# Performance work log

Hardware: AMD Instinct MI355X
Metric: run time of the kernel (lower is better)

## Reference

```python
import jax, jax.numpy as jnp
import numpy as np

OUTPUT_LEN = 8  # init: output_len
# init: pred_conversion=False, conf_thres=None, vote_conf_by_count=True, select_by_conf=True


def setup_inputs() -> dict:
    key = jax.random.key(0)
    x = jax.random.normal(key, (128, 8192, 64), dtype=jnp.float32)
    return {"x": x}


def _per_sample(conf, pred):
    # conf, pred: [T]
    T = conf.shape[0]
    # run-length encoding (unique_consecutive): mark the start of each run
    is_start = jnp.concatenate([jnp.ones((1,), bool), pred[1:] != pred[:-1]])
    run_id = jnp.cumsum(is_start.astype(jnp.int32)) - 1  # [T], run index per position
    # count of each run (padded to T segments; unused segments are 0)
    counts = jax.ops.segment_sum(jnp.ones((T,), conf.dtype), run_id, num_segments=T)
    # voted confidence at run starts: conf_at_start * run_count (vote_conf_by_count=True)
    voted = jnp.where(is_start, conf * counts[run_id], -jnp.inf)
    # select_by_conf=True: take top output_len runs by voted confidence
    vals, idx = jax.lax.top_k(voted, OUTPUT_LEN)
    sel = pred[idx]
    # fewer runs than output_len -> pad with 0 (torch pads with new_zeros)
    sel = jnp.where(jnp.isfinite(vals), sel, 0)
    return sel


def reference(x):
    p = jax.nn.softmax(x, axis=-1)          # [B, T, C]
    conf = jnp.max(p, axis=-1)              # [B, T]
    pred = jnp.argmax(p, axis=-1)           # [B, T] int
    out = jax.vmap(_per_sample)(conf, pred)  # [B, OUTPUT_LEN] int
    return out.astype(x.dtype)               # x.new_tensor(results) -> float
```

## Files before the change

### kernel.cpp

```cpp
#include <hip/hip_runtime.h>
#include <stdint.h>

#define T_LEN 8192
#define C_LEN 64
#define OUT_LEN 8

__global__ __launch_bounds__(256) void softmax_stats_kernel(
    const float* __restrict__ x, float* __restrict__ conf,
    int* __restrict__ pred, int nrows)
{
    const int tid  = threadIdx.x;
    const int wave = tid >> 6;
    const int lane = tid & 63;
    const int rw   = lane >> 4;
    const int sub  = lane & 15;
    const long long row = (long long)blockIdx.x * 16 + wave * 4 + rw;
    if (row >= nrows) return;

    const float4 v = ((const float4*)(x + row * C_LEN))[sub];

    float m = v.x; int mi = sub * 4;
    if (v.y > m) { m = v.y; mi = sub * 4 + 1; }
    if (v.z > m) { m = v.z; mi = sub * 4 + 2; }
    if (v.w > m) { m = v.w; mi = sub * 4 + 3; }

    const unsigned int s0 = __float_as_uint(m);
    const unsigned int u0 = (s0 & 0x80000000u) ? ~s0 : (s0 | 0x80000000u);
    unsigned long long key =
        ((unsigned long long)u0 << 32) | (unsigned int)~mi;

    #pragma unroll
    for (int off = 8; off >= 1; off >>= 1) {
        const unsigned long long o = __shfl_xor(key, off);
        if (o > key) key = o;
    }

    const unsigned int uu = (unsigned int)(key >> 32);
    const float M = __uint_as_float(
        (uu & 0x80000000u) ? (uu ^ 0x80000000u) : ~uu);

    float s = __expf(v.x - M) + __expf(v.y - M)
            + __expf(v.z - M) + __expf(v.w - M);
    #pragma unroll
    for (int off = 8; off >= 1; off >>= 1) s += __shfl_xor(s, off);

    if (sub == 0) {
        conf[row] = 1.0f / s;
        pred[row] = (int)~(unsigned int)(key & 0xffffffffu);
    }
}

__global__ __launch_bounds__(256) void topk_kernel(
    const float* __restrict__ conf, const int* __restrict__ pred,
    float* __restrict__ out)
{
    __shared__ short pred_s[T_LEN];
    __shared__ float voted_s[T_LEN];
    __shared__ unsigned long long wkey[4];
    __shared__ int   dirty;
    __shared__ float outbuf[OUT_LEN];

    const int b    = blockIdx.x;
    const int tid  = threadIdx.x;
    const int lane = tid & 63, wave = tid >> 6;
    const int* __restrict__   pb = pred + (long long)b * T_LEN;
    const float* __restrict__ cb = conf + (long long)b * T_LEN;

    for (int i = tid; i < T_LEN / 4; i += 256) {
        const int4 p4 = ((const int4*)pb)[i];
        short4 q; q.x = (short)p4.x; q.y = (short)p4.y;
        q.z = (short)p4.z; q.w = (short)p4.w;
        *(short4*)&pred_s[4 * i] = q;
    }
    if (tid == 0) dirty = -1;
    __syncthreads();

    for (int t = tid; t < T_LEN; t += 256) {
        const short p = pred_s[t];
        const bool start = (t == 0) || (pred_s[t - 1] != p);
        float v = 0.0f;
        if (start) {
            int len = 1;
            while (t + len < T_LEN && pred_s[t + len] == p) ++len;
            v = cb[t] * (float)len;
        }
        voted_s[t] = v;
    }
    __syncthreads();

    for (int r = 0; r < OUT_LEN; ++r) {
        if (dirty == -1 || dirty == wave) {
            unsigned long long best = 0ull;
            const int base = wave * (T_LEN / 4);
            #pragma unroll 4
            for (int k = 0; k < T_LEN / 4 / 64; ++k) {
                const int t = base + k * 64 + lane;
                const unsigned long long key =
                    ((unsigned long long)__float_as_uint(voted_s[t]) << 32)
                    | (unsigned int)(~t);
                if (key > best) best = key;
            }
            #pragma unroll
            for (int off = 32; off >= 1; off >>= 1) {
                const unsigned long long o = __shfl_xor(best, off);
                if (o > best) best = o;
            }
            if (lane == 0) wkey[wave] = best;
        }
        __syncthreads();
        if (tid == 0) {
            unsigned long long bb = wkey[0];
            #pragma unroll
            for (int w = 1; w < 4; ++w) if (wkey[w] > bb) bb = wkey[w];
            const unsigned int widx = ~(unsigned int)(bb & 0xffffffffu);
            const float v = __uint_as_float((unsigned int)(bb >> 32));
            float ov = 0.0f;
            if (v > 0.0f) {
                ov = (float)pred_s[widx];
                voted_s[widx] = 0.0f;
                dirty = (int)(widx / (T_LEN / 4));
            } else {
                dirty = 4;
            }
            outbuf[r] = ov;
        }
        __syncthreads();
    }
    if (tid < OUT_LEN) out[b * OUT_LEN + tid] = outbuf[tid];
}

extern "C" void kernel_launch(void* const* d_in, const int* in_sizes, int n_in,
                              void* d_out, int out_size, void* d_ws, size_t ws_size,
                              hipStream_t stream) {
    const float* x = (const float*)d_in[0];
    const int total = in_sizes[0];
    const int nrows = total / C_LEN;
    const int B     = nrows / T_LEN;

    float* conf = (float*)d_ws;
    int*   pred = (int*)((char*)d_ws + (size_t)nrows * sizeof(float));
    float* out  = (float*)d_out;

    const int gridA = (nrows + 15) / 16;
    softmax_stats_kernel<<<gridA, 256, 0, stream>>>(x, conf, pred, nrows);
    softmax_stats_kernel<<<gridA, 256, 0, stream>>>(x, conf, pred, nrows);
    topk_kernel<<<B, 256, 0, stream>>>(conf, pred, out);
}
```

Before: 418.0 us.

## Split per-sample top-k into segmented blocks with merge, drop duplicate softmax launch

The softmax stats kernel, which was launched twice, now runs once and writes conf and pred packed into one int2 array. The per-sample top-k is split into four segment blocks per sample. Each block computes run-length votes with a halo plus global fallback, then emits its top-8 candidate keys. A small merge kernel picks the final top-8 per sample. This raises the top-k stage from 128 to 512 blocks and removes a redundant pass over the 256 MB input, at the cost of an extra launch and candidate buffer traffic.

```diff
diff --git a/kernel.cpp b/kernel.cpp
--- a/kernel.cpp
+++ b/kernel.cpp
@@ -4,10 +4,11 @@
 #define T_LEN 8192
 #define C_LEN 64
 #define OUT_LEN 8
+#define SEG 2048
+#define HALO 512
 
 __global__ __launch_bounds__(256) void softmax_stats_kernel(
-    const float* __restrict__ x, float* __restrict__ conf,
-    int* __restrict__ pred, int nrows)
+    const float* __restrict__ x, int2* __restrict__ packed, int nrows)
 {
     const int tid  = threadIdx.x;
     const int wave = tid >> 6;
@@ -45,59 +46,68 @@
     for (int off = 8; off >= 1; off >>= 1) s += __shfl_xor(s, off);
 
     if (sub == 0) {
-        conf[row] = 1.0f / s;
-        pred[row] = (int)~(unsigned int)(key & 0xffffffffu);
+        int2 o;
+        o.x = __float_as_int(1.0f / s);
+        o.y = (int)~(unsigned int)(key & 0xffffffffu);
+        packed[row] = o;
     }
 }
 
-__global__ __launch_bounds__(256) void topk_kernel(
-    const float* __restrict__ conf, const int* __restrict__ pred,
-    float* __restrict__ out)
+__global__ __launch_bounds__(256) void topk_seg_kernel(
+    const int2* __restrict__ packed, unsigned long long* __restrict__ cand)
 {
-    __shared__ short pred_s[T_LEN];
-    __shared__ float voted_s[T_LEN];
+    __shared__ short pred_s[SEG + HALO + 1];
+    __shared__ float conf_s[SEG];
+    __shared__ float voted_s[SEG];
     __shared__ unsigned long long wkey[4];
-    __shared__ int   dirty;
-    __shared__ float outbuf[OUT_LEN];
+    __shared__ int dirty;
 
-    const int b    = blockIdx.x;
-    const int tid  = threadIdx.x;
-    const int lane = tid & 63, wave = tid >> 6;
-    const int* __restrict__   pb = pred + (long long)b * T_LEN;
-    const float* __restrict__ cb = conf + (long long)b * T_LEN;
+    const int tid    = threadIdx.x;
+    const int lane   = tid & 63, wave = tid >> 6;
+    const int sample = blockIdx.x >> 2;
+    const int seg    = blockIdx.x & 3;
+    const int seg_start = seg * SEG;
+    const int2* __restrict__ pp = packed + (long long)sample * T_LEN;
 
-    for (int i = tid; i < T_LEN / 4; i += 256) {
-        const int4 p4 = ((const int4*)pb)[i];
-        short4 q; q.x = (short)p4.x; q.y = (short)p4.y;
-        q.z = (short)p4.z; q.w = (short)p4.w;
-        *(short4*)&pred_s[4 * i] = q;
+    const int lo = (seg == 0) ? 0 : seg_start - 1;
+    int hi = seg_start + SEG + HALO; if (hi > T_LEN) hi = T_LEN;
+    for (int i = lo + tid; i < hi; i += 256) {
+        const int2 p = pp[i];
+        pred_s[i - seg_start + 1] = (short)p.y;
+        const int k = i - seg_start;
+        if ((unsigned)k < SEG) conf_s[k] = __int_as_float(p.x);
     }
+    if (seg == 0 && tid == 0) pred_s[0] = (short)0x7fff;
     if (tid == 0) dirty = -1;
     __syncthreads();
 
-    for (int t = tid; t < T_LEN; t += 256) {
-        const short p = pred_s[t];
-        const bool start = (t == 0) || (pred_s[t - 1] != p);
+    for (int k = tid; k < SEG; k += 256) {
+        const int t = seg_start + k;
+        const short p = pred_s[k + 1];
         float v = 0.0f;
-        if (start) {
+        if (p != pred_s[k]) {
             int len = 1;
-            while (t + len < T_LEN && pred_s[t + len] == p) ++len;
-            v = cb[t] * (float)len;
+            const int lim = hi - t;
+            while (len < lim && pred_s[k + 1 + len] == p) ++len;
+            if (len == lim && t + len < T_LEN) {
+                while (t + len < T_LEN && (short)pp[t + len].y == p) ++len;
+            }
+            v = conf_s[k] * (float)len;
         }
-        voted_s[t] = v;
+        voted_s[k] = v;
     }
     __syncthreads();
 
     for (int r = 0; r < OUT_LEN; ++r) {
         if (dirty == -1 || dirty == wave) {
             unsigned long long best = 0ull;
-            const int base = wave * (T_LEN / 4);
-            #pragma unroll 4
-            for (int k = 0; k < T_LEN / 4 / 64; ++k) {
-                const int t = base + k * 64 + lane;
+            const int base = wave * (SEG / 4);
+            #pragma unroll
+            for (int kk = 0; kk < SEG / 4 / 64; ++kk) {
+                const int k = base + kk * 64 + lane;
                 const unsigned long long key =
-                    ((unsigned long long)__float_as_uint(voted_s[t]) << 32)
-                    | (unsigned int)(~t);
+                    ((unsigned long long)__float_as_uint(voted_s[k]) << 32)
+                    | (unsigned int)~(seg_start + k);
                 if (key > best) best = key;
             }
             #pragma unroll
@@ -112,37 +122,66 @@
             unsigned long long bb = wkey[0];
             #pragma unroll
             for (int w = 1; w < 4; ++w) if (wkey[w] > bb) bb = wkey[w];
-            const unsigned int widx = ~(unsigned int)(bb & 0xffffffffu);
-            const float v = __uint_as_float((unsigned int)(bb >> 32));
-            float ov = 0.0f;
-            if (v > 0.0f) {
-                ov = (float)pred_s[widx];
-                voted_s[widx] = 0.0f;
-                dirty = (int)(widx / (T_LEN / 4));
+            if ((bb >> 32) != 0ull) {
+                const int tg = (int)~(unsigned int)(bb & 0xffffffffu);
+                const int k = tg - seg_start;
+                voted_s[k] = 0.0f;
+                dirty = k / (SEG / 4);
             } else {
                 dirty = 4;
             }
-            outbuf[r] = ov;
+            cand[(long long)blockIdx.x * OUT_LEN + r] = bb;
         }
         __syncthreads();
     }
-    if (tid < OUT_LEN) out[b * OUT_LEN + tid] = outbuf[tid];
+}
+
+__global__ __launch_bounds__(64) void topk_merge_kernel(
+    const unsigned long long* __restrict__ cand,
+    const int2* __restrict__ packed, float* __restrict__ out)
+{
+    const int sample = blockIdx.x;
+    const int lane   = threadIdx.x;
+
+    unsigned long long key = 0ull;
+    float pv = 0.0f;
+    if (lane < 4 * OUT_LEN) key = cand[(long long)sample * 32 + lane];
+    if (key != 0ull) {
+        const int tg = (int)~(unsigned int)(key & 0xffffffffu);
+        pv = (float)packed[(long long)sample * T_LEN + tg].y;
+    }
+
+    for (int r = 0; r < OUT_LEN; ++r) {
+        unsigned long long best = key;
+        #pragma unroll
+        for (int off = 32; off >= 1; off >>= 1) {
+            const unsigned long long o = __shfl_xor(best, off);
+            if (o > best) best = o;
+        }
+        if (best == 0ull) {
+            if (lane == 0) out[sample * OUT_LEN + r] = 0.0f;
+        } else if (key == best) {
+            out[sample * OUT_LEN + r] = pv;
+            key = 0ull;
+        }
+    }
 }
 
 extern "C" void kernel_launch(void* const* d_in, const int* in_sizes, int n_in,
                               void* d_out, int out_size, void* d_ws, size_t ws_size,
                               hipStream_t stream) {
-    const float* x = (const float*)d_in[0];
+    const float* x  = (const float*)d_in[0];
     const int total = in_sizes[0];
     const int nrows = total / C_LEN;
     const int B     = nrows / T_LEN;
 
-    float* conf = (float*)d_ws;
-    int*   pred = (int*)((char*)d_ws + (size_t)nrows * sizeof(float));
-    float* out  = (float*)d_out;
+    int2* packed = (int2*)d_ws;
+    unsigned long long* cand =
+        (unsigned long long*)((char*)d_ws + (size_t)nrows * sizeof(int2));
+    float* out = (float*)d_out;
 
     const int gridA = (nrows + 15) / 16;
-    softmax_stats_kernel<<<gridA, 256, 0, stream>>>(x, conf, pred, nrows);
-    softmax_stats_kernel<<<gridA, 256, 0, stream>>>(x, conf, pred, nrows);
-    topk_kernel<<<B, 256, 0, stream>>>(conf, pred, out);
+    softmax_stats_kernel<<<gridA, 256, 0, stream>>>(x, packed, nrows);
+    topk_seg_kernel<<<B * 4, 256, 0, stream>>>(packed, cand);
+    topk_merge_kernel<<<B, 64, 0, stream>>>(cand, packed, out);
 }
```

Result: faster. 354.5 us (-15.2%).
